# Performance work log

Hardware: AMD Instinct MI355X
Metric: run time of the kernel (lower is better)

The kernel has to match this reference:

```python
import jax, jax.numpy as jnp
import numpy as np
from jax import lax

T_NO = 200
SUB_NO = 16
E_NO = 2000
I_NO = 500
T_DATA = 20000
COS_BASIS_NO = 16
COS_SHIFT = 1.0
COS_SCALE = 4.0


def make_cos_basis(T_no):
    # [cos_basis_no, T_no] raised-cosine basis, matches torch loop exactly
    i = jnp.arange(COS_BASIS_NO, dtype=jnp.float32)[:, None]
    phi = (jnp.pi / 2.0) * i
    x = jnp.arange(T_no, dtype=jnp.float32)[None, :]
    raw = COS_SCALE * jnp.log(x + COS_SHIFT)
    basis = 0.5 * jnp.cos(raw - phi) + 0.5
    return jnp.where((raw < phi - jnp.pi) | (raw > phi + jnp.pi), 0.0, basis)


@jax.custom_vjp
def step(x):
    # torch.heaviside(x, 0): 1 for x>0, 0 for x<=0
    return jnp.where(x > 0, 1.0, 0.0).astype(x.dtype)

def _step_fwd(x):
    return step(x), x

def _step_bwd(x, g):
    return (g / (1.0 + jnp.abs(x)) ** 2,)

step.defvjp(_step_fwd, _step_bwd)


def _depthwise_causal(pad, kern_flipped):
    # pad: [T_data+T_no, sub], kern_flipped: [sub, T_no] (already flipped, torch-style)
    lhs = pad.T[None]                      # [1, sub, L]
    rhs = kern_flipped[:, None, :]          # [sub, 1, T_no]
    out = lax.conv_general_dilated(lhs, rhs, (1,), 'VALID',
                                   dimension_numbers=('NCH', 'OIH', 'NCH'),
                                   feature_group_count=SUB_NO)
    return out[0].T                         # [T_data+1, sub]


def _srm_forward(S_e, S_i, C_den, C_syn_e, C_syn_i, Tau_syn_e, Tau_syn_i,
                 W_syn_e, W_syn_i, Delta_syn_e, Delta_syn_i, Tau_spk, W_spk,
                 W_hist, Theta):
    T_no = T_NO
    cos_basis = make_cos_basis(T_no)
    syn_e = S_e @ C_syn_e.T                 # [T_data, sub]
    syn_i = S_i @ C_syn_i.T

    t = jnp.arange(T_no, dtype=jnp.float32)[None, :]
    t_e = jnp.maximum(t - jnp.exp(Delta_syn_e)[:, None], 0.0)
    t_i = jnp.maximum(t - jnp.exp(Delta_syn_i)[:, None], 0.0)
    tt_e = t_e / jnp.exp(Tau_syn_e)[:, None]
    tt_i = t_i / jnp.exp(Tau_syn_i)[:, None]
    e_kern = tt_e * jnp.exp(-tt_e) * jnp.exp(W_syn_e)[:, None]       # [sub, T_no]
    i_kern = -tt_i * jnp.exp(-tt_i) * jnp.exp(W_syn_i)[:, None]

    zpad = jnp.zeros((T_no, SUB_NO), syn_e.dtype)
    filt_e = _depthwise_causal(jnp.concatenate([zpad, syn_e], 0), jnp.flip(e_kern, 1))[:-1]
    filt_i = _depthwise_causal(jnp.concatenate([zpad, syn_i], 0), jnp.flip(i_kern, 1))[:-1]
    syn = filt_e + filt_i                   # [T_data, sub]

    tt_spk = t / jnp.exp(Tau_spk)[:, None]
    spk_kern = tt_spk * jnp.exp(-tt_spk) * jnp.exp(W_spk)[:, None]   # [sub, T_no]
    hist_kern = W_hist @ cos_basis                                    # [sub, T_no]
    spk_kern_f = jnp.flip(spk_kern, 1)
    hist_kern_f = jnp.flip(hist_kern, 1)

    def step_fn(buf, syn_t):
        # buf: [T_no, sub] rolling spike history, buf[-1] = most recent
        hist_in = jnp.einsum('ts,st->s', buf, hist_kern_f)
        spk_in_raw = jnp.einsum('ts,st->s', buf, spk_kern_f)
        spk_in = C_den @ spk_in_raw
        sub_in = hist_in + spk_in + syn_t + Theta
        s = step(sub_in)
        return jnp.concatenate([buf[1:], s[None]], 0), s

    buf0 = jnp.zeros((T_no, SUB_NO), syn.dtype)
    _, spk_out = lax.scan(step_fn, buf0, syn)   # [T_data, sub]

    out_filters = jnp.vstack([e_kern, i_kern, spk_kern, hist_kern])  # [4*sub, T_no]
    return spk_out, out_filters


def setup_inputs() -> dict:
    key = jax.random.key(0)
    ks = jax.random.split(key, 10)
    # sparse-ish spike trains
    S_e = (jax.random.uniform(ks[0], (T_DATA, E_NO)) < 0.02).astype(jnp.float32)
    S_i = (jax.random.uniform(ks[1], (T_DATA, I_NO)) < 0.02).astype(jnp.float32)
    # each synapse maps to exactly one subunit
    C_syn_e = jax.nn.one_hot(jax.random.randint(ks[2], (E_NO,), 0, SUB_NO), SUB_NO).T.astype(jnp.float32)
    C_syn_i = jax.nn.one_hot(jax.random.randint(ks[3], (I_NO,), 0, SUB_NO), SUB_NO).T.astype(jnp.float32)
    C_den = (jax.random.uniform(ks[4], (SUB_NO, SUB_NO)) < 0.15).astype(jnp.float32)
    ones = jnp.ones(SUB_NO, jnp.float32)
    return {
        'S_e': S_e, 'S_i': S_i, 'C_den': C_den, 'C_syn_e': C_syn_e, 'C_syn_i': C_syn_i,
        'Tau_syn_e': ones * 1.0, 'Tau_syn_i': ones * 1.0,
        'W_syn_e': ones * 0.5, 'W_syn_i': ones * 0.5,
        'Delta_syn_e': ones * 1.0, 'Delta_syn_i': ones * 1.0,
        'Tau_spk': ones * 1.0, 'W_spk': ones * -1.0,
        'W_hist': 0.1 * jax.random.normal(ks[5], (SUB_NO, COS_BASIS_NO), jnp.float32),
        'Theta': -0.5 * ones + 0.1 * jax.random.normal(ks[6], (SUB_NO,), jnp.float32),
    }


def reference(S_e, S_i, C_den, C_syn_e, C_syn_i, Tau_syn_e, Tau_syn_i, W_syn_e,
              W_syn_i, Delta_syn_e, Delta_syn_i, Tau_spk, W_spk, W_hist, Theta):
    return _srm_forward(S_e, S_i, C_den, C_syn_e, C_syn_i, Tau_syn_e, Tau_syn_i,
                        W_syn_e, W_syn_i, Delta_syn_e, Delta_syn_i, Tau_spk, W_spk,
                        W_hist, Theta)
```

## Files before the change

kernel.cpp:

```cpp
#include <hip/hip_runtime.h>

#ifndef M_PI
#define M_PI 3.14159265358979323846
#endif

#define T_DATA 20000
#define E_NO_C 2000
#define I_NO_C 500
#define SUB 16
#define TNO 200
#define NGRP 5000
#define NSUP 2500

typedef float v2f __attribute__((ext_vector_type(2)));

template <bool B> struct BC { static constexpr bool v = B; };

__device__ __forceinline__ float quad_sum(float v) {
  int a = __builtin_amdgcn_mov_dpp(__float_as_int(v), 177, 0xf, 0xf, true);
  v += __int_as_float(a);
  int b = __builtin_amdgcn_mov_dpp(__float_as_int(v), 78, 0xf, 0xf, true);
  v += __int_as_float(b);
  return v;
}

__device__ __forceinline__ void bar_sync() {
  asm volatile("s_waitcnt lgkmcnt(0)" ::: "memory");
  __builtin_amdgcn_s_barrier();
  asm volatile("" ::: "memory");
}

__global__ void filters_k(const float* __restrict__ Tau_e, const float* __restrict__ Tau_i,
                          const float* __restrict__ W_e,  const float* __restrict__ W_i,
                          const float* __restrict__ D_e,  const float* __restrict__ D_i,
                          const float* __restrict__ Tau_spk, const float* __restrict__ W_spk,
                          const float* __restrict__ W_hist,
                          float* __restrict__ filt_out) {
  int id = blockIdx.x * blockDim.x + threadIdx.x;
  if (id >= 64 * TNO) return;
  int r = id / TNO, x = id % TNO;
  int s = r & 15, kind = r >> 4;
  double xd = (double)x;
  double val;
  if (kind == 0) {
    double te = xd - exp((double)D_e[s]); te = te > 0.0 ? te : 0.0;
    double tt = te / exp((double)Tau_e[s]);
    val = tt * exp(-tt) * exp((double)W_e[s]);
  } else if (kind == 1) {
    double ti = xd - exp((double)D_i[s]); ti = ti > 0.0 ? ti : 0.0;
    double tt = ti / exp((double)Tau_i[s]);
    val = -tt * exp(-tt) * exp((double)W_i[s]);
  } else if (kind == 2) {
    double tt = xd / exp((double)Tau_spk[s]);
    val = tt * exp(-tt) * exp((double)W_spk[s]);
  } else {
    double raw = 4.0 * log(xd + 1.0);
    double acc = 0.0;
    for (int i = 0; i < 16; ++i) {
      double phi = (M_PI / 2.0) * (double)i;
      double b = (raw < phi - M_PI || raw > phi + M_PI) ? 0.0
                                                        : (0.5 * cos(raw - phi) + 0.5);
      acc += (double)W_hist[s * 16 + i] * b;
    }
    val = acc;
  }
  filt_out[id] = (float)val;
}

#define ETILE 500
__global__ __launch_bounds__(256) void synmm_k(const float* __restrict__ S,
                                               const float* __restrict__ C,
                                               float* __restrict__ out, int E) {
  __shared__ __align__(16) float Cs[16][ETILE];
  int tid = threadIdx.x;
  int s = tid & 15, tt = tid >> 4;
  long t = (long)blockIdx.x * 16 + tt;
  const float* Srow = S + t * E;
  float acc = 0.f;
  for (int tb = 0; tb < E; tb += ETILE) {
    __syncthreads();
    for (int i = tid; i < 16 * ETILE; i += 256) {
      int s2 = i / ETILE, k2 = i - s2 * ETILE;
      Cs[s2][k2] = C[(long)s2 * E + tb + k2];
    }
    __syncthreads();
    const float* Crow = &Cs[s][0];
    const float* Sp = Srow + tb;
#pragma unroll 2
    for (int e = 0; e < ETILE; e += 4) {
      float4 a = *(const float4*)(Sp + e);
      float4 c = *(const float4*)(Crow + e);
      acc = fmaf(a.x, c.x, acc); acc = fmaf(a.y, c.y, acc);
      acc = fmaf(a.z, c.z, acc); acc = fmaf(a.w, c.w, acc);
    }
  }
  out[t * 16 + s] = acc;
}

__global__ void conv_k(const float* __restrict__ syn_e, const float* __restrict__ syn_i,
                       const float* __restrict__ filt, const float* __restrict__ Theta,
                       float* __restrict__ synTh) {
  __shared__ float ek[16][201];
  __shared__ float ik[16][201];
  int tid = threadIdx.x;
  for (int idx = tid; idx < 16 * TNO; idx += 256) {
    ek[idx / TNO][idx % TNO] = filt[idx];
    ik[idx / TNO][idx % TNO] = filt[16 * TNO + idx];
  }
  __syncthreads();
  int s = tid & 15, tt = tid >> 4;
  int t = blockIdx.x * 16 + tt;
  float acc = Theta[s];
  if (t >= TNO) {
#pragma unroll 4
    for (int j = 0; j < TNO; ++j) {
      int u = t - 1 - j;
      acc += ek[s][j] * syn_e[u * 16 + s] + ik[s][j] * syn_i[u * 16 + s];
    }
  } else {
    for (int j = 0; j < t; ++j) {
      int u = t - 1 - j;
      acc += ek[s][j] * syn_e[u * 16 + s] + ik[s][j] * syn_i[u * 16 + s];
    }
  }
  synTh[t * 16 + s] = acc;
}

__global__ __launch_bounds__(512, 1) void scan15_k(const float* __restrict__ synTh,
                                                   const float* __restrict__ filt,
                                                   const float* __restrict__ C_den,
                                                   const float* __restrict__ Tau_spk,
                                                   const float* __restrict__ W_spk,
                                                   float* __restrict__ spk_out) {
  __shared__ __align__(16) float ring[16][452];
  __shared__ __align__(16) float oPartF[2][5][2][64];
  __shared__ __align__(16) float farsumF[2][2][64];
  __shared__ __align__(16) float synStage[2][4][16][20];
  const int tid = threadIdx.x;
  const int widx = tid >> 6;
  const int l = tid & 63;
  const int s = l & 15, q = l >> 4;

  for (int i = tid; i < 16 * 452; i += 512) (&ring[0][0])[i] = 0.f;
  for (int i = tid; i < 2 * 5 * 2 * 64; i += 512) (&oPartF[0][0][0][0])[i] = 0.f;
  for (int i = tid; i < 2 * 2 * 64; i += 512) (&farsumF[0][0][0])[i] = 0.f;
  __syncthreads();
  if (widx == 7) {
    int e0 = 4 * l;
    float4 v = *(const float4*)&synTh[e0];
    int t0 = e0 >> 4, s0 = e0 & 15;
    int g = t0 >> 2, K = t0 & 3;
    synStage[0][g & 3][s0 + 0][K] = v.x;
    synStage[0][g & 3][s0 + 1][K] = v.y;
    synStage[0][g & 3][s0 + 2][K] = v.z;
    synStage[0][g & 3][s0 + 3][K] = v.w;
  }
  __syncthreads();

  if (widx == 0) {
    const float* hrow = filt + (48 + s) * TNO;
    float hk[15];
#pragma unroll
    for (int i = 0; i < 15; ++i) hk[i] = hrow[i];

    float t0v = Tau_spk[0], w0v = W_spk[0];
    bool okrow = (Tau_spk[s] == t0v) && (W_spk[s] == w0v);
    unsigned cd = 0u;
#pragma unroll
    for (int j = 0; j < 16; ++j) {
      float cv = C_den[s * 16 + j];
      okrow = okrow && (cv == 0.f || cv == 1.f);
      cd |= (cv != 0.f) ? (1u << j) : 0u;
    }
    const bool uni = (bool)__all((int)okrow);

    const double tau  = exp((double)Tau_spk[s]);
    const double aa   = exp(-1.0 / tau);
    const double c2a  = exp((double)W_spk[s]) * aa / tau;
    const double twoa = 2.0 * aa;
    const double na2  = -aa * aa;

    double twoa4[4], na24[4], c2a4[4], yd0a[4], yd1a[4];
    float cden4[4];
#pragma unroll
    for (int r = 0; r < 4; ++r) {
      int j = 4 * q + r;
      double tj = exp((double)Tau_spk[j]);
      double aj = exp(-1.0 / tj);
      twoa4[r] = 2.0 * aj; na24[r] = -aj * aj;
      c2a4[r]  = exp((double)W_spk[j]) * aj / tj;
      yd0a[r] = 0.0; yd1a[r] = 0.0;
      cden4[r] = C_den[s * 16 + j];
    }

    double zA = 0.0, zB = 0.0;
    float mixu = 0.f, mix1 = 0.f;
    float sgPrev = 0.f;
    float S0 = 0.f, S1 = 0.f, S2 = 0.f, S3 = 0.f;
    float cA0 = 0.f, cA1 = 0.f, cA2 = 0.f, cA3 = 0.f;
    float ccA0 = 0.f, ccA1 = 0.f, ccA2 = 0.f, ccA3 = 0.f;
    float nrA0 = 0.f, nrA1 = 0.f, nrA2 = 0.f, nrA3 = 0.f;
    float ccB0 = 0.f, ccB1 = 0.f, ccB2 = 0.f, ccB3 = 0.f;
    float nrB0 = 0.f, nrB1 = 0.f, nrB2 = 0.f, nrB3 = 0.f;

    float4 fsA_r = *(const float4*)&farsumF[0][0][4 * s];
    float4 fsB_r = *(const float4*)&farsumF[0][1][4 * s];
    float4 synA_r = *(const float4*)&synStage[0][0][s][0];
    float4 synB_r = *(const float4*)&synStage[0][1][s][0];

#define STEP(SGD, PRE, SGOUT)                                                 \
    {                                                                         \
      float sub = fmaf(hk[0], (SGD), (PRE));                                  \
      unsigned long long bal = __ballot(sub > 0.f);                           \
      float sg = sub > 0.f ? 1.f : 0.f;                                       \
      if constexpr (UNI) {                                                    \
        unsigned xm = (unsigned)bal & cd;              \
        double zc = fma(twoa, zB, fma(na2, zA, c2a * (double)__popc(xm)));    \
        zA = zB; zB = zc;                                                     \
        mixu = (float)zA;                                                     \
      } else {                                                                \
        unsigned mk = (unsigned)bal & 0xFFFFu;                                \
        float p = 0.f;                                                        \
        _Pragma("unroll")                                                     \
        for (int r = 0; r < 4; ++r) {                                         \
          double xr = (double)((mk >> (4 * q + r)) & 1u);                     \
          double y2 = fma(twoa4[r], yd1a[r], fma(na24[r], yd0a[r], c2a4[r] * xr)); \
          yd0a[r] = yd1a[r]; yd1a[r] = y2;                                    \
          p = fmaf(cden4[r], (float)y2, p);                                   \
        }                                                                     \
        p += __shfl_xor(p, 16); p += __shfl_xor(p, 32);                       \
        float mixn = mix1; mix1 = p;                                          \
        mixu = mixn;                                                          \
      }                                                                       \
      (SGOUT) = sg;                                                           \
    }

    auto scan_loop = [&](auto uc) {
      constexpr bool UNI = decltype(uc)::v;
      for (int M = 0; M < NSUP; ++M) {
        float ocA0 = ((nrA0 + fsA_r.x) + (synA_r.x + cA0)) + ccA0;
        float ocA1 = ((nrA1 + fsA_r.y) + (synA_r.y + cA1)) + ccA1;
        float ocA2 = ((nrA2 + fsA_r.z) + (synA_r.z + cA2)) + ccA2;
        float ocA3 = ((nrA3 + fsA_r.w) + (synA_r.w + cA3)) + ccA3;

        float SA0, SA1, SA2, SA3;
        STEP(sgPrev, ocA0 + mixu, SA0)
        float pend2 = hk[1] * SA0;
        float pend3 = hk[2] * SA0;
        STEP(SA0, ocA1 + mixu, SA1)
        pend3 = fmaf(hk[1], SA1, pend3);
        STEP(SA1, (ocA2 + mixu) + pend2, SA2)
        STEP(SA2, (ocA3 + mixu) + pend3, SA3)

        if (l < 16) {
          int u = (8 * M) & 255;
          float4 w0; w0.x = SA0; w0.y = SA1; w0.z = SA2; w0.w = SA3;
          *(float4*)&ring[s][u] = w0;
          if (u < 192) *(float4*)&ring[s][u + 256] = w0;
        }

        float cB0 = fmaf(hk[1], SA2, fmaf(hk[2], SA1, hk[3] * SA0));
        float cB1 = fmaf(hk[1], SA3, fmaf(hk[2], SA2, fmaf(hk[3], SA1, hk[4] * SA0)));
        float cB2 = fmaf(hk[2], SA3, fmaf(hk[3], SA2, fmaf(hk[4], SA1, hk[5] * SA0)));
        float cB3 = fmaf(hk[3], SA3, fmaf(hk[4], SA2, fmaf(hk[5], SA1, hk[6] * SA0)));

        float ocB0 = ((nrB0 + fsB_r.x) + (synB_r.x + cB0)) + ccB0;
        float ocB1 = ((nrB1 + fsB_r.y) + (synB_r.y + cB1)) + ccB1;
        float ocB2 = ((nrB2 + fsB_r.z) + (synB_r.z + cB2)) + ccB2;
        float ocB3 = ((nrB3 + fsB_r.w) + (synB_r.w + cB3)) + ccB3;

        float SB0, SB1, SB2, SB3;
        STEP(SA3, ocB0 + mixu, SB0)
        float pend2b = hk[1] * SB0;
        float pend3b = hk[2] * SB0;
        STEP(SB0, ocB1 + mixu, SB1)
        pend3b = fmaf(hk[1], SB1, pend3b);
        STEP(SB1, (ocB2 + mixu) + pend2b, SB2)
        STEP(SB2, (ocB3 + mixu) + pend3b, SB3)

        if (l < 16) {
          int u = (8 * M + 4) & 255;
          float4 w0; w0.x = SB0; w0.y = SB1; w0.z = SB2; w0.w = SB3;
          *(float4*)&ring[s][u] = w0;
          if (u < 192) *(float4*)&ring[s][u + 256] = w0;
        }

        bar_sync();

        {
          const int Mn = M + 1;
          const int gAn = 2 * Mn, gBn = 2 * Mn + 1;
          fsA_r = *(const float4*)&farsumF[Mn & 1][0][4 * s];
          fsB_r = *(const float4*)&farsumF[Mn & 1][1][4 * s];
          synA_r = *(const float4*)&synStage[(gAn >> 2) & 1][gAn & 3][s][0];
          synB_r = *(const float4*)&synStage[(gBn >> 2) & 1][gBn & 3][s][0];
        }

        cA0 = fmaf(hk[1], SB2, fmaf(hk[2], SB1, hk[3] * SB0));
        cA1 = fmaf(hk[1], SB3, fmaf(hk[2], SB2, fmaf(hk[3], SB1, hk[4] * SB0)));
        cA2 = fmaf(hk[2], SB3, fmaf(hk[3], SB2, fmaf(hk[4], SB1, hk[5] * SB0)));
        cA3 = fmaf(hk[3], SB3, fmaf(hk[4], SB2, fmaf(hk[5], SB1, hk[6] * SB0)));
        ccA0 = fmaf(hk[7], SA0, fmaf(hk[6], SA1, fmaf(hk[5], SA2, hk[4] * SA3)));
        ccA1 = fmaf(hk[8], SA0, fmaf(hk[7], SA1, fmaf(hk[6], SA2, hk[5] * SA3)));
        ccA2 = fmaf(hk[9], SA0, fmaf(hk[8], SA1, fmaf(hk[7], SA2, hk[6] * SA3)));
        ccA3 = fmaf(hk[10], SA0, fmaf(hk[9], SA1, fmaf(hk[8], SA2, hk[7] * SA3)));
        ccB0 = fmaf(hk[7], SB0, fmaf(hk[6], SB1, fmaf(hk[5], SB2, hk[4] * SB3)));
        ccB1 = fmaf(hk[8], SB0, fmaf(hk[7], SB1, fmaf(hk[6], SB2, hk[5] * SB3)));
        ccB2 = fmaf(hk[9], SB0, fmaf(hk[8], SB1, fmaf(hk[7], SB2, hk[6] * SB3)));
        ccB3 = fmaf(hk[10], SB0, fmaf(hk[9], SB1, fmaf(hk[8], SB2, hk[7] * SB3)));
        nrA0 = fmaf(hk[11], S0, fmaf(hk[10], S1, fmaf(hk[9], S2, hk[8] * S3)));
        nrA1 = fmaf(hk[12], S0, fmaf(hk[11], S1, fmaf(hk[10], S2, hk[9] * S3)));
        nrA2 = fmaf(hk[13], S0, fmaf(hk[12], S1, fmaf(hk[11], S2, hk[10] * S3)));
        nrA3 = fmaf(hk[14], S0, fmaf(hk[13], S1, fmaf(hk[12], S2, hk[11] * S3)));
        nrB0 = fmaf(hk[11], SA0, fmaf(hk[10], SA1, fmaf(hk[9], SA2, hk[8] * SA3)));
        nrB1 = fmaf(hk[12], SA0, fmaf(hk[11], SA1, fmaf(hk[10], SA2, hk[9] * SA3)));
        nrB2 = fmaf(hk[13], SA0, fmaf(hk[12], SA1, fmaf(hk[11], SA2, hk[10] * SA3)));
        nrB3 = fmaf(hk[14], SA0, fmaf(hk[13], SA1, fmaf(hk[12], SA2, hk[11] * SA3)));

        S0 = SB0; S1 = SB1; S2 = SB2; S3 = SB3;
        sgPrev = SB3;
        bar_sync();
      }
    };
    if (uni) scan_loop(BC<true>{});
    else     scan_loop(BC<false>{});
#undef STEP
  } else if (widx == 4) {
    for (int M = 0; M < NSUP; ++M) {
      bar_sync();
      bar_sync();
    }
  } else if (widx == 7) {
    const int s2 = l >> 2, K = l & 3;
    const float* hrow = filt + (48 + s2) * TNO;
    float hc5[32];
#pragma unroll
    for (int x = 0; x < 32; ++x) hc5[x] = hrow[12 + K + x];

    for (int M = 0; M < NSUP; ++M) {
      float4 vv;
      const bool doStage = (M & 1) && (2 * M + 2 < NGRP);
      if (doStage) vv = *(const float4*)&synTh[(2 * M + 2) * 64 + 4 * l];

      int pos0 = (8 * M - 36) & 255;
      const float4* rp = (const float4*)&ring[s2][pos0];
      float e[36];
#pragma unroll
      for (int i = 0; i < 9; ++i) {
        float4 R = rp[i];
        e[4 * i + 0] = R.x; e[4 * i + 1] = R.y; e[4 * i + 2] = R.z; e[4 * i + 3] = R.w;
      }
      float f5v[2];
#pragma unroll
      for (int p = 0; p < 2; ++p) {
        float oo[4];
#pragma unroll
        for (int c = 0; c < 4; ++c) {
          v2f p01, p23, p45, p67, PR7, PR5, PR3, PR1;
          int ofs = 4 * p + 8 * c;
          p01.x = e[ofs + 0]; p01.y = e[ofs + 1];
          p23.x = e[ofs + 2]; p23.y = e[ofs + 3];
          p45.x = e[ofs + 4]; p45.y = e[ofs + 5];
          p67.x = e[ofs + 6]; p67.y = e[ofs + 7];
          PR7.x = hc5[31 - 8 * c]; PR7.y = hc5[30 - 8 * c];
          PR5.x = hc5[29 - 8 * c]; PR5.y = hc5[28 - 8 * c];
          PR3.x = hc5[27 - 8 * c]; PR3.y = hc5[26 - 8 * c];
          PR1.x = hc5[25 - 8 * c]; PR1.y = hc5[24 - 8 * c];
          v2f a = PR7 * p01; a += PR5 * p23; a += PR3 * p45; a += PR1 * p67;
          oo[c] = a.x + a.y;
        }
        f5v[p] = (oo[0] + oo[1]) + (oo[2] + oo[3]);
      }

      const int slot = M & 1, wbuf = (M + 1) & 1;
      float t0e = oPartF[slot][0][0][l] + oPartF[slot][1][0][l];
      float t1e = oPartF[slot][2][0][l] + oPartF[slot][3][0][l];
      float t2e = oPartF[slot][4][0][l] + f5v[0];
      farsumF[wbuf][0][l] = (t0e + t1e) + t2e;
      float t0o = oPartF[slot][0][1][l] + oPartF[slot][1][1][l];
      float t1o = oPartF[slot][2][1][l] + oPartF[slot][3][1][l];
      float t2o = oPartF[slot][4][1][l] + f5v[1];
      farsumF[wbuf][1][l] = (t0o + t1o) + t2o;

      if (doStage) {
        int e0 = (2 * M + 2) * 64 + 4 * l;
        int t0i = e0 >> 4, s0 = e0 & 15;
        int g = t0i >> 2, Kk = t0i & 3;
        int buf = (g >> 2) & 1;
        synStage[buf][g & 3][s0 + 0][Kk] = vv.x;
        synStage[buf][g & 3][s0 + 1][Kk] = vv.y;
        synStage[buf][g & 3][s0 + 2][Kk] = vv.z;
        synStage[buf][g & 3][s0 + 3][Kk] = vv.w;
      }

      bar_sync();

      if ((M & 3) == 0 && M > 0) {
        int n = 2 * M;
        int We = (4 * n - 1) & 255;
        if (We < 191) We += 256;
        int base2 = We - 31;
#pragma unroll
        for (int r = 0; r < 2; ++r) {
          int eo = 64 * (n - 8) + 256 * r + 4 * l;
          int t0i = eo >> 4, s0 = eo & 15;
          int pos = base2 + (t0i - 4 * (n - 8));
          float4 w;
          w.x = ring[s0 + 0][pos]; w.y = ring[s0 + 1][pos];
          w.z = ring[s0 + 2][pos]; w.w = ring[s0 + 3][pos];
          *(float4*)&spk_out[eo] = w;
        }
      }
      bar_sync();
    }
    {
      int n = NGRP;
      int We = (4 * n - 1) & 255;
      if (We < 191) We += 256;
      int base2 = We - 31;
#pragma unroll
      for (int r = 0; r < 2; ++r) {
        int eo = 64 * (n - 8) + 256 * r + 4 * l;
        int t0i = eo >> 4, s0 = eo & 15;
        int pos = base2 + (t0i - 4 * (n - 8));
        float4 w;
        w.x = ring[s0 + 0][pos]; w.y = ring[s0 + 1][pos];
        w.z = ring[s0 + 2][pos]; w.w = ring[s0 + 3][pos];
        *(float4*)&spk_out[eo] = w;
      }
    }
  } else {
    const int f = (widx < 4) ? (widx - 1) : (widx - 2);
    const int s2 = l >> 2, qq = l & 3;
    const float* hrow = filt + (48 + s2) * TNO;
    const int base = 196 - 32 * f - 8 * qq;
    float ca[11];
#pragma unroll
    for (int m = 0; m < 11; ++m) {
      int hidx = base + m;
      ca[m] = (hidx <= 199) ? hrow[hidx] : 0.f;
    }
    v2f pr[11];
    pr[0].x = 0.f; pr[0].y = 0.f;
#pragma unroll
    for (int m = 1; m < 11; ++m) { pr[m].x = ca[m]; pr[m].y = ca[m - 1]; }

    for (int M = 0; M < NSUP; ++M) {
      int W0 = (8 * M - 188 + 32 * f + 8 * qq) & 255;
      const float4* rp = (const float4*)&ring[s2][W0];
      float4 V0 = rp[0], V1 = rp[1], V2 = rp[2];
      v2f p01, p23, p45, p67, q01, q23, q45, q67;
      p01.x = V0.x; p01.y = V0.y; p23.x = V0.z; p23.y = V0.w;
      p45.x = V1.x; p45.y = V1.y; p67.x = V1.z; p67.y = V1.w;
      q01.x = V1.x; q01.y = V1.y; q23.x = V1.z; q23.y = V1.w;
      q45.x = V2.x; q45.y = V2.y; q67.x = V2.z; q67.y = V2.w;
      float o0, o1, o2, o3, o4, o5, o6, o7;
      { v2f a = pr[7] * p01;  a += pr[5] * p23; a += pr[3] * p45; a += pr[1] * p67; o0 = a.x + a.y; }
      { v2f a = pr[8] * p01;  a += pr[6] * p23; a += pr[4] * p45; a += pr[2] * p67; o1 = a.x + a.y; }
      { v2f a = pr[9] * p01;  a += pr[7] * p23; a += pr[5] * p45; a += pr[3] * p67; o2 = a.x + a.y; }
      { v2f a = pr[10] * p01; a += pr[8] * p23; a += pr[6] * p45; a += pr[4] * p67; o3 = a.x + a.y; }
      { v2f a = pr[7] * q01;  a += pr[5] * q23; a += pr[3] * q45; a += pr[1] * q67; o4 = a.x + a.y; }
      { v2f a = pr[8] * q01;  a += pr[6] * q23; a += pr[4] * q45; a += pr[2] * q67; o5 = a.x + a.y; }
      { v2f a = pr[9] * q01;  a += pr[7] * q23; a += pr[5] * q45; a += pr[3] * q67; o6 = a.x + a.y; }
      { v2f a = pr[10] * q01; a += pr[8] * q23; a += pr[6] * q45; a += pr[4] * q67; o7 = a.x + a.y; }
      o0 = quad_sum(o0); o1 = quad_sum(o1); o2 = quad_sum(o2); o3 = quad_sum(o3);
      o4 = quad_sum(o4); o5 = quad_sum(o5); o6 = quad_sum(o6); o7 = quad_sum(o7);
      float myoE = (qq == 0) ? o0 : (qq == 1) ? o1 : (qq == 2) ? o2 : o3;
      float myoO = (qq == 0) ? o4 : (qq == 1) ? o5 : (qq == 2) ? o6 : o7;
      const int slot = (M + 1) & 1;
      oPartF[slot][f][0][l] = myoE;
      oPartF[slot][f][1][l] = myoO;
      bar_sync();
      bar_sync();
    }
  }
}

extern "C" void kernel_launch(void* const* d_in, const int* in_sizes, int n_in,
                              void* d_out, int out_size, void* d_ws, size_t ws_size,
                              hipStream_t stream) {
  const float* S_e     = (const float*)d_in[0];
  const float* S_i     = (const float*)d_in[1];
  const float* C_den   = (const float*)d_in[2];
  const float* C_syn_e = (const float*)d_in[3];
  const float* C_syn_i = (const float*)d_in[4];
  const float* Tau_e   = (const float*)d_in[5];
  const float* Tau_i   = (const float*)d_in[6];
  const float* W_e     = (const float*)d_in[7];
  const float* W_i     = (const float*)d_in[8];
  const float* D_e     = (const float*)d_in[9];
  const float* D_i     = (const float*)d_in[10];
  const float* Tau_spk = (const float*)d_in[11];
  const float* W_spk   = (const float*)d_in[12];
  const float* W_hist  = (const float*)d_in[13];
  const float* Theta   = (const float*)d_in[14];

  float* out     = (float*)d_out;
  float* spk_out = out;
  float* filt    = out + 320000;

  float* ws    = (float*)d_ws;
  float* syn_e = ws;
  float* syn_i = ws + 320000;
  float* synTh = ws + 640000;

  filters_k<<<50, 256, 0, stream>>>(Tau_e, Tau_i, W_e, W_i, D_e, D_i,
                                    Tau_spk, W_spk, W_hist, filt);
  synmm_k<<<1250, 256, 0, stream>>>(S_e, C_syn_e, syn_e, E_NO_C);
  synmm_k<<<1250, 256, 0, stream>>>(S_i, C_syn_i, syn_i, I_NO_C);
  conv_k<<<1250, 256, 0, stream>>>(syn_e, syn_i, filt, Theta, synTh);
  scan15_k<<<1, 512, 0, stream>>>(synTh, filt, C_den, Tau_spk, W_spk, spk_out);
}
```

Before: 1.924 ms.

## Relax barrier waits and precompute next-step offsets before barrier in scan

Splits the barrier helper into a draining variant and a raw variant that skips the LDS wait-count, using the raw one where no prior LDS writes need to be visible. The serial scan wave now finishes combining the next iteration's partial sums right after the first barrier, so the start of the next step carries less dependent arithmetic. oPartF is re-laid out so the even/odd partials are written and read as one float2. The serial recurrence loop should get shorter, at the cost of careful reasoning about whether skipping the LDS wait is safe at each barrier.

```diff
diff --git a/kernel.cpp b/kernel.cpp
--- a/kernel.cpp
+++ b/kernel.cpp
@@ -24,8 +24,13 @@
   return v;
 }
 
-__device__ __forceinline__ void bar_sync() {
+__device__ __forceinline__ void bar_drain() {
   asm volatile("s_waitcnt lgkmcnt(0)" ::: "memory");
+  __builtin_amdgcn_s_barrier();
+  asm volatile("" ::: "memory");
+}
+__device__ __forceinline__ void bar_raw() {
+  asm volatile("" ::: "memory");
   __builtin_amdgcn_s_barrier();
   asm volatile("" ::: "memory");
 }
@@ -126,14 +131,14 @@
   synTh[t * 16 + s] = acc;
 }
 
-__global__ __launch_bounds__(512, 1) void scan15_k(const float* __restrict__ synTh,
+__global__ __launch_bounds__(512, 1) void scan16_k(const float* __restrict__ synTh,
                                                    const float* __restrict__ filt,
                                                    const float* __restrict__ C_den,
                                                    const float* __restrict__ Tau_spk,
                                                    const float* __restrict__ W_spk,
                                                    float* __restrict__ spk_out) {
   __shared__ __align__(16) float ring[16][452];
-  __shared__ __align__(16) float oPartF[2][5][2][64];
+  __shared__ __align__(16) float oPartF[2][5][64][2];
   __shared__ __align__(16) float farsumF[2][2][64];
   __shared__ __align__(16) float synStage[2][4][16][20];
   const int tid = threadIdx.x;
@@ -142,7 +147,7 @@
   const int s = l & 15, q = l >> 4;
 
   for (int i = tid; i < 16 * 452; i += 512) (&ring[0][0])[i] = 0.f;
-  for (int i = tid; i < 2 * 5 * 2 * 64; i += 512) (&oPartF[0][0][0][0])[i] = 0.f;
+  for (int i = tid; i < 2 * 5 * 64 * 2; i += 512) (&oPartF[0][0][0][0])[i] = 0.f;
   for (int i = tid; i < 2 * 2 * 64; i += 512) (&farsumF[0][0][0])[i] = 0.f;
   __syncthreads();
   if (widx == 7) {
@@ -197,16 +202,25 @@
     float mixu = 0.f, mix1 = 0.f;
     float sgPrev = 0.f;
     float S0 = 0.f, S1 = 0.f, S2 = 0.f, S3 = 0.f;
-    float cA0 = 0.f, cA1 = 0.f, cA2 = 0.f, cA3 = 0.f;
-    float ccA0 = 0.f, ccA1 = 0.f, ccA2 = 0.f, ccA3 = 0.f;
-    float nrA0 = 0.f, nrA1 = 0.f, nrA2 = 0.f, nrA3 = 0.f;
-    float ccB0 = 0.f, ccB1 = 0.f, ccB2 = 0.f, ccB3 = 0.f;
-    float nrB0 = 0.f, nrB1 = 0.f, nrB2 = 0.f, nrB3 = 0.f;
-
-    float4 fsA_r = *(const float4*)&farsumF[0][0][4 * s];
-    float4 fsB_r = *(const float4*)&farsumF[0][1][4 * s];
-    float4 synA_r = *(const float4*)&synStage[0][0][s][0];
-    float4 synB_r = *(const float4*)&synStage[0][1][s][0];
+
+    float ocA0, ocA1, ocA2, ocA3;
+    float uB0, uB1, uB2, uB3;
+    float sB0, sB1, sB2, sB3;
+    float ccBk0, ccBk1, ccBk2, ccBk3;
+    {
+      float4 fsA_r = *(const float4*)&farsumF[0][0][4 * s];
+      float4 fsB_r = *(const float4*)&farsumF[0][1][4 * s];
+      float4 synA_r = *(const float4*)&synStage[0][0][s][0];
+      float4 synB_r = *(const float4*)&synStage[0][1][s][0];
+      float z0 = 0.f;
+      ocA0 = ((z0 + fsA_r.x) + (synA_r.x + z0)) + z0;
+      ocA1 = ((z0 + fsA_r.y) + (synA_r.y + z0)) + z0;
+      ocA2 = ((z0 + fsA_r.z) + (synA_r.z + z0)) + z0;
+      ocA3 = ((z0 + fsA_r.w) + (synA_r.w + z0)) + z0;
+      uB0 = z0 + fsB_r.x; uB1 = z0 + fsB_r.y; uB2 = z0 + fsB_r.z; uB3 = z0 + fsB_r.w;
+      sB0 = synB_r.x; sB1 = synB_r.y; sB2 = synB_r.z; sB3 = synB_r.w;
+      ccBk0 = z0; ccBk1 = z0; ccBk2 = z0; ccBk3 = z0;
+    }
 
 #define STEP(SGD, PRE, SGOUT)                                                 \
     {                                                                         \
@@ -238,11 +252,6 @@
     auto scan_loop = [&](auto uc) {
       constexpr bool UNI = decltype(uc)::v;
       for (int M = 0; M < NSUP; ++M) {
-        float ocA0 = ((nrA0 + fsA_r.x) + (synA_r.x + cA0)) + ccA0;
-        float ocA1 = ((nrA1 + fsA_r.y) + (synA_r.y + cA1)) + ccA1;
-        float ocA2 = ((nrA2 + fsA_r.z) + (synA_r.z + cA2)) + ccA2;
-        float ocA3 = ((nrA3 + fsA_r.w) + (synA_r.w + cA3)) + ccA3;
-
         float SA0, SA1, SA2, SA3;
         STEP(sgPrev, ocA0 + mixu, SA0)
         float pend2 = hk[1] * SA0;
@@ -263,11 +272,10 @@
         float cB1 = fmaf(hk[1], SA3, fmaf(hk[2], SA2, fmaf(hk[3], SA1, hk[4] * SA0)));
         float cB2 = fmaf(hk[2], SA3, fmaf(hk[3], SA2, fmaf(hk[4], SA1, hk[5] * SA0)));
         float cB3 = fmaf(hk[3], SA3, fmaf(hk[4], SA2, fmaf(hk[5], SA1, hk[6] * SA0)));
-
-        float ocB0 = ((nrB0 + fsB_r.x) + (synB_r.x + cB0)) + ccB0;
-        float ocB1 = ((nrB1 + fsB_r.y) + (synB_r.y + cB1)) + ccB1;
-        float ocB2 = ((nrB2 + fsB_r.z) + (synB_r.z + cB2)) + ccB2;
-        float ocB3 = ((nrB3 + fsB_r.w) + (synB_r.w + cB3)) + ccB3;
+        float ocB0 = (uB0 + (sB0 + cB0)) + ccBk0;
+        float ocB1 = (uB1 + (sB1 + cB1)) + ccBk1;
+        float ocB2 = (uB2 + (sB2 + cB2)) + ccBk2;
+        float ocB3 = (uB3 + (sB3 + cB3)) + ccBk3;
 
         float SB0, SB1, SB2, SB3;
         STEP(SA3, ocB0 + mixu, SB0)
@@ -285,41 +293,48 @@
           if (u < 192) *(float4*)&ring[s][u + 256] = w0;
         }
 
-        bar_sync();
-
-        {
-          const int Mn = M + 1;
-          const int gAn = 2 * Mn, gBn = 2 * Mn + 1;
-          fsA_r = *(const float4*)&farsumF[Mn & 1][0][4 * s];
-          fsB_r = *(const float4*)&farsumF[Mn & 1][1][4 * s];
-          synA_r = *(const float4*)&synStage[(gAn >> 2) & 1][gAn & 3][s][0];
-          synB_r = *(const float4*)&synStage[(gBn >> 2) & 1][gBn & 3][s][0];
-        }
-
-        cA0 = fmaf(hk[1], SB2, fmaf(hk[2], SB1, hk[3] * SB0));
-        cA1 = fmaf(hk[1], SB3, fmaf(hk[2], SB2, fmaf(hk[3], SB1, hk[4] * SB0)));
-        cA2 = fmaf(hk[2], SB3, fmaf(hk[3], SB2, fmaf(hk[4], SB1, hk[5] * SB0)));
-        cA3 = fmaf(hk[3], SB3, fmaf(hk[4], SB2, fmaf(hk[5], SB1, hk[6] * SB0)));
-        ccA0 = fmaf(hk[7], SA0, fmaf(hk[6], SA1, fmaf(hk[5], SA2, hk[4] * SA3)));
-        ccA1 = fmaf(hk[8], SA0, fmaf(hk[7], SA1, fmaf(hk[6], SA2, hk[5] * SA3)));
-        ccA2 = fmaf(hk[9], SA0, fmaf(hk[8], SA1, fmaf(hk[7], SA2, hk[6] * SA3)));
-        ccA3 = fmaf(hk[10], SA0, fmaf(hk[9], SA1, fmaf(hk[8], SA2, hk[7] * SA3)));
-        ccB0 = fmaf(hk[7], SB0, fmaf(hk[6], SB1, fmaf(hk[5], SB2, hk[4] * SB3)));
-        ccB1 = fmaf(hk[8], SB0, fmaf(hk[7], SB1, fmaf(hk[6], SB2, hk[5] * SB3)));
-        ccB2 = fmaf(hk[9], SB0, fmaf(hk[8], SB1, fmaf(hk[7], SB2, hk[6] * SB3)));
-        ccB3 = fmaf(hk[10], SB0, fmaf(hk[9], SB1, fmaf(hk[8], SB2, hk[7] * SB3)));
-        nrA0 = fmaf(hk[11], S0, fmaf(hk[10], S1, fmaf(hk[9], S2, hk[8] * S3)));
-        nrA1 = fmaf(hk[12], S0, fmaf(hk[11], S1, fmaf(hk[10], S2, hk[9] * S3)));
-        nrA2 = fmaf(hk[13], S0, fmaf(hk[12], S1, fmaf(hk[11], S2, hk[10] * S3)));
-        nrA3 = fmaf(hk[14], S0, fmaf(hk[13], S1, fmaf(hk[12], S2, hk[11] * S3)));
-        nrB0 = fmaf(hk[11], SA0, fmaf(hk[10], SA1, fmaf(hk[9], SA2, hk[8] * SA3)));
-        nrB1 = fmaf(hk[12], SA0, fmaf(hk[11], SA1, fmaf(hk[10], SA2, hk[9] * SA3)));
-        nrB2 = fmaf(hk[13], SA0, fmaf(hk[12], SA1, fmaf(hk[11], SA2, hk[10] * SA3)));
-        nrB3 = fmaf(hk[14], SA0, fmaf(hk[13], SA1, fmaf(hk[12], SA2, hk[11] * SA3)));
+        bar_raw();
+
+        const int Mn = M + 1;
+        const int gAn = 2 * Mn, gBn = 2 * Mn + 1;
+        float4 fsA_r = *(const float4*)&farsumF[Mn & 1][0][4 * s];
+        float4 fsB_r = *(const float4*)&farsumF[Mn & 1][1][4 * s];
+        float4 synA_r = *(const float4*)&synStage[(gAn >> 2) & 1][gAn & 3][s][0];
+        float4 synB_r = *(const float4*)&synStage[(gBn >> 2) & 1][gBn & 3][s][0];
+
+        float cA0 = fmaf(hk[1], SB2, fmaf(hk[2], SB1, hk[3] * SB0));
+        float cA1 = fmaf(hk[1], SB3, fmaf(hk[2], SB2, fmaf(hk[3], SB1, hk[4] * SB0)));
+        float cA2 = fmaf(hk[2], SB3, fmaf(hk[3], SB2, fmaf(hk[4], SB1, hk[5] * SB0)));
+        float cA3 = fmaf(hk[3], SB3, fmaf(hk[4], SB2, fmaf(hk[5], SB1, hk[6] * SB0)));
+        float ccA0 = fmaf(hk[7], SA0, fmaf(hk[6], SA1, fmaf(hk[5], SA2, hk[4] * SA3)));
+        float ccA1 = fmaf(hk[8], SA0, fmaf(hk[7], SA1, fmaf(hk[6], SA2, hk[5] * SA3)));
+        float ccA2 = fmaf(hk[9], SA0, fmaf(hk[8], SA1, fmaf(hk[7], SA2, hk[6] * SA3)));
+        float ccA3 = fmaf(hk[10], SA0, fmaf(hk[9], SA1, fmaf(hk[8], SA2, hk[7] * SA3)));
+        float nrA0 = fmaf(hk[11], S0, fmaf(hk[10], S1, fmaf(hk[9], S2, hk[8] * S3)));
+        float nrA1 = fmaf(hk[12], S0, fmaf(hk[11], S1, fmaf(hk[10], S2, hk[9] * S3)));
+        float nrA2 = fmaf(hk[13], S0, fmaf(hk[12], S1, fmaf(hk[11], S2, hk[10] * S3)));
+        float nrA3 = fmaf(hk[14], S0, fmaf(hk[13], S1, fmaf(hk[12], S2, hk[11] * S3)));
+        float ccB0 = fmaf(hk[7], SB0, fmaf(hk[6], SB1, fmaf(hk[5], SB2, hk[4] * SB3)));
+        float ccB1 = fmaf(hk[8], SB0, fmaf(hk[7], SB1, fmaf(hk[6], SB2, hk[5] * SB3)));
+        float ccB2 = fmaf(hk[9], SB0, fmaf(hk[8], SB1, fmaf(hk[7], SB2, hk[6] * SB3)));
+        float ccB3 = fmaf(hk[10], SB0, fmaf(hk[9], SB1, fmaf(hk[8], SB2, hk[7] * SB3)));
+        float nrB0 = fmaf(hk[11], SA0, fmaf(hk[10], SA1, fmaf(hk[9], SA2, hk[8] * SA3)));
+        float nrB1 = fmaf(hk[12], SA0, fmaf(hk[11], SA1, fmaf(hk[10], SA2, hk[9] * SA3)));
+        float nrB2 = fmaf(hk[13], SA0, fmaf(hk[12], SA1, fmaf(hk[11], SA2, hk[10] * SA3)));
+        float nrB3 = fmaf(hk[14], SA0, fmaf(hk[13], SA1, fmaf(hk[12], SA2, hk[11] * SA3)));
+
+        ocA0 = ((nrA0 + fsA_r.x) + (synA_r.x + cA0)) + ccA0;
+        ocA1 = ((nrA1 + fsA_r.y) + (synA_r.y + cA1)) + ccA1;
+        ocA2 = ((nrA2 + fsA_r.z) + (synA_r.z + cA2)) + ccA2;
+        ocA3 = ((nrA3 + fsA_r.w) + (synA_r.w + cA3)) + ccA3;
+        uB0 = nrB0 + fsB_r.x; uB1 = nrB1 + fsB_r.y;
+        uB2 = nrB2 + fsB_r.z; uB3 = nrB3 + fsB_r.w;
+        sB0 = synB_r.x; sB1 = synB_r.y; sB2 = synB_r.z; sB3 = synB_r.w;
+        ccBk0 = ccB0; ccBk1 = ccB1; ccBk2 = ccB2; ccBk3 = ccB3;
 
         S0 = SB0; S1 = SB1; S2 = SB2; S3 = SB3;
         sgPrev = SB3;
-        bar_sync();
+        bar_drain();
       }
     };
     if (uni) scan_loop(BC<true>{});
@@ -327,8 +342,8 @@
 #undef STEP
   } else if (widx == 4) {
     for (int M = 0; M < NSUP; ++M) {
-      bar_sync();
-      bar_sync();
+      bar_raw();
+      bar_raw();
     }
   } else if (widx == 7) {
     const int s2 = l >> 2, K = l & 3;
@@ -373,13 +388,18 @@
       }
 
       const int slot = M & 1, wbuf = (M + 1) & 1;
-      float t0e = oPartF[slot][0][0][l] + oPartF[slot][1][0][l];
-      float t1e = oPartF[slot][2][0][l] + oPartF[slot][3][0][l];
-      float t2e = oPartF[slot][4][0][l] + f5v[0];
+      float2 pa = *(const float2*)&oPartF[slot][0][l][0];
+      float2 pb = *(const float2*)&oPartF[slot][1][l][0];
+      float2 pc = *(const float2*)&oPartF[slot][2][l][0];
+      float2 pd = *(const float2*)&oPartF[slot][3][l][0];
+      float2 pe = *(const float2*)&oPartF[slot][4][l][0];
+      float t0e = pa.x + pb.x;
+      float t1e = pc.x + pd.x;
+      float t2e = pe.x + f5v[0];
       farsumF[wbuf][0][l] = (t0e + t1e) + t2e;
-      float t0o = oPartF[slot][0][1][l] + oPartF[slot][1][1][l];
-      float t1o = oPartF[slot][2][1][l] + oPartF[slot][3][1][l];
-      float t2o = oPartF[slot][4][1][l] + f5v[1];
+      float t0o = pa.y + pb.y;
+      float t1o = pc.y + pd.y;
+      float t2o = pe.y + f5v[1];
       farsumF[wbuf][1][l] = (t0o + t1o) + t2o;
 
       if (doStage) {
@@ -393,7 +413,7 @@
         synStage[buf][g & 3][s0 + 3][Kk] = vv.w;
       }
 
-      bar_sync();
+      bar_drain();
 
       if ((M & 3) == 0 && M > 0) {
         int n = 2 * M;
@@ -411,7 +431,7 @@
           *(float4*)&spk_out[eo] = w;
         }
       }
-      bar_sync();
+      bar_drain();
     }
     {
       int n = NGRP;
@@ -468,10 +488,10 @@
       float myoE = (qq == 0) ? o0 : (qq == 1) ? o1 : (qq == 2) ? o2 : o3;
       float myoO = (qq == 0) ? o4 : (qq == 1) ? o5 : (qq == 2) ? o6 : o7;
       const int slot = (M + 1) & 1;
-      oPartF[slot][f][0][l] = myoE;
-      oPartF[slot][f][1][l] = myoO;
-      bar_sync();
-      bar_sync();
+      float2 w2; w2.x = myoE; w2.y = myoO;
+      *(float2*)&oPartF[slot][f][l][0] = w2;
+      bar_raw();
+      bar_drain();
     }
   }
 }
@@ -509,5 +529,5 @@
   synmm_k<<<1250, 256, 0, stream>>>(S_e, C_syn_e, syn_e, E_NO_C);
   synmm_k<<<1250, 256, 0, stream>>>(S_i, C_syn_i, syn_i, I_NO_C);
   conv_k<<<1250, 256, 0, stream>>>(syn_e, syn_i, filt, Theta, synTh);
-  scan15_k<<<1, 512, 0, stream>>>(synTh, filt, C_den, Tau_spk, W_spk, spk_out);
-}
+  scan16_k<<<1, 512, 0, stream>>>(synTh, filt, C_den, Tau_spk, W_spk, spk_out);
+}
```

New measurement: 1.868 ms. -2.9%, faster.
